# Kernel tuning notes

Measured on AMD Instinct MI355X. Metric: run time of the kernel, lower is better.

The kernel has to match this reference:

```python
import jax, jax.numpy as jnp
import numpy as np

B, H, W, C = 8, 64, 64, 64
DI = 2 * C   # d_inner = ssm_ratio * hidden_dim
N = 1        # ssm_d_state
K = 4        # scan directions
R = 4        # dt_rank = ceil(C/16)
EPS = 1e-5


def _ln(x, w, b):
    mu = x.mean(-1, keepdims=True)
    var = x.var(-1, keepdims=True)
    return (x - mu) / jnp.sqrt(var + EPS) * w + b


def _vss(x, p):
    (norm1_w, norm1_b, in_proj_w, conv_w, x_proj_w, dt_projs_w, dt_projs_b,
     A_logs, Ds, out_norm_w, out_norm_b, out_proj_w, norm2_w, norm2_b,
     fc1_w, fc1_b, fc2_w, fc2_b) = p
    # ---- SS2D branch (forward_type='v2') ----
    h = _ln(x, norm1_w, norm1_b)
    xz = h @ in_proj_w.T                      # (B,H,W,2*DI)
    xc, z = jnp.split(xz, 2, axis=-1)
    z = jax.nn.silu(z)
    xc = xc.transpose(0, 3, 1, 2)             # (B,DI,H,W)
    xc = jax.lax.conv_general_dilated(
        xc, conv_w, (1, 1), [(1, 1), (1, 1)], feature_group_count=DI,
        dimension_numbers=('NCHW', 'OIHW', 'NCHW'))  # depthwise 3x3, no bias
    xc = jax.nn.silu(xc)
    L = H * W
    # CrossScan: row-major, col-major, and their reverses
    x0 = xc.reshape(B, DI, L)
    x1 = xc.transpose(0, 1, 3, 2).reshape(B, DI, L)
    xs = jnp.stack([x0, x1, x0[..., ::-1], x1[..., ::-1]], axis=1)  # (B,K,DI,L)
    x_dbl = jnp.einsum('bkdl,kcd->bkcl', xs, x_proj_w)
    dts, Bs, Cs = x_dbl[:, :, :R], x_dbl[:, :, R:R + N], x_dbl[:, :, R + N:]
    delta = jax.nn.softplus(jnp.einsum('bkrl,kdr->bkdl', dts, dt_projs_w)
                            + dt_projs_b[None, :, :, None])          # (B,K,DI,L)
    A = -jnp.exp(A_logs).reshape(K, DI, N)
    # diagonal linear recurrence h_t = a_t*h_{t-1} + b_t via associative scan
    a = jnp.exp(delta[..., None] * A[None, :, :, None, :])           # (B,K,DI,L,N)
    b = delta[..., None] * Bs.transpose(0, 1, 3, 2)[:, :, None] * xs[..., None]
    def comb(c1, c2):
        a1, b1 = c1
        a2, b2 = c2
        return a1 * a2, b1 * a2 + b2
    _, hst = jax.lax.associative_scan(comb, (a, b), axis=3)          # (B,K,DI,L,N)
    ys = jnp.einsum('bkdln,bknl->bkdl', hst, Cs) \
         + Ds.reshape(K, DI)[None, :, :, None] * xs
    # CrossMerge
    ys = ys[:, :2] + ys[:, 2:, :, ::-1]
    y = ys[:, 0] + ys[:, 1].reshape(B, DI, W, H).transpose(0, 1, 3, 2).reshape(B, DI, L)
    y = y.transpose(0, 2, 1).reshape(B, H, W, DI)
    y = _ln(y, out_norm_w, out_norm_b)
    y = (y * z) @ out_proj_w.T
    x = x + y
    # ---- MLP branch ----
    h2 = _ln(x, norm2_w, norm2_b)
    h2 = jax.nn.gelu(h2 @ fc1_w.T + fc1_b, approximate=False)
    return x + (h2 @ fc2_w.T + fc2_b)


def setup_inputs():
    key = jax.random.key(0)
    ks = jax.random.split(key, 16)
    g = lambda i, shape, s=0.02: jax.random.normal(ks[i], shape, jnp.float32) * s
    return {
        'mag': jax.random.normal(ks[0], (B, H, W, C), jnp.float32),
        'phase': jax.random.normal(ks[1], (B, H, W, C), jnp.float32),
        'norm1_w': jnp.ones((2, C)), 'norm1_b': jnp.zeros((2, C)),
        'in_proj_w': g(2, (2, 2 * DI, C)),
        'conv_w': g(3, (2, DI, 1, 3, 3), 0.1),
        'x_proj_w': g(4, (2, K, R + 2 * N, DI)),
        'dt_projs_w': g(5, (2, K, DI, R), 0.1),
        'dt_projs_b': g(6, (2, K, DI), 0.1),
        'A_logs': g(7, (2, K * DI, N), 1.0),
        'Ds': jnp.ones((2, K * DI)),
        'out_norm_w': jnp.ones((2, DI)), 'out_norm_b': jnp.zeros((2, DI)),
        'out_proj_w': g(8, (2, C, DI)),
        'norm2_w': jnp.ones((2, C)), 'norm2_b': jnp.zeros((2, C)),
        'fc1_w': g(9, (2, 4 * C, C)), 'fc1_b': jnp.zeros((2, 4 * C)),
        'fc2_w': g(10, (2, C, 4 * C)), 'fc2_b': jnp.zeros((2, C)),
    }


def reference(mag, phase, norm1_w, norm1_b, in_proj_w, conv_w, x_proj_w,
              dt_projs_w, dt_projs_b, A_logs, Ds, out_norm_w, out_norm_b,
              out_proj_w, norm2_w, norm2_b, fc1_w, fc1_b, fc2_w, fc2_b):
    params = (norm1_w, norm1_b, in_proj_w, conv_w, x_proj_w, dt_projs_w,
              dt_projs_b, A_logs, Ds, out_norm_w, out_norm_b, out_proj_w,
              norm2_w, norm2_b, fc1_w, fc1_b, fc2_w, fc2_b)
    outs = jax.vmap(_vss)(jnp.stack([mag, phase]), params)  # branch dim = 2
    s = outs[0] + outs[1]
    return (s, s)
```

## Files before the change

kernel.cpp:

```cpp
#include <hip/hip_runtime.h>
#include <math.h>

#define LL   4096
#define DI   128
#define CC   64
#define BB   8
#define KK   4
#define LB   32768
#define NPIX 2097152
#define EPSF 1e-5f

#define OFF_XCIN   ((size_t)0)
#define OFF_XCONV  ((size_t)4194304)
#define OFF_XCONVT ((size_t)8388608)
#define OFF_Z      ((size_t)12582912)
#define OFF_Y      ((size_t)16777216)
#define OFF_YT     ((size_t)20971520)
#define OFF_XDBL   ((size_t)25165824)
#define ISTRIDE    ((size_t)25952256)
#define OFF_YCOMBT OFF_XCIN
#define OFF_XNEW   OFF_YT
#define OFF_SB     OFF_Y
#define OFF_WB     (OFF_Y + (size_t)2097152)
#define WB_IPW 0
#define WB_OPW 16384
#define WB_F1W 24576
#define WB_F2W 40960
#define WB_TOT 57344

typedef short v8s __attribute__((ext_vector_type(8)));
typedef float v4f __attribute__((ext_vector_type(4)));

__device__ __forceinline__ float fexp_(float x){ return __expf(x); }
__device__ __forceinline__ float silu_(float x){ return __fdividef(x, 1.f+__expf(-x)); }
__device__ __forceinline__ float softplusf_(float x){
  return fmaxf(x,0.f) + __logf(1.f + __expf(-fabsf(x)));
}
__device__ __forceinline__ float geluf_(float x){ return 0.5f*x*(1.f+erff(x*0.70710678118f)); }
__device__ __forceinline__ short bf16_(float x){
  unsigned u = __float_as_uint(x);
  u += 0x7FFF + ((u>>16)&1);
  return (short)(u>>16);
}
__device__ __forceinline__ float bf2f_(short s){
  return __uint_as_float(((unsigned)(unsigned short)s)<<16);
}

#define LD16(dst, ptr) { const float4* p4_=(const float4*)(ptr);                 \
  float4 v0_=p4_[0], v1_=p4_[1], v2_=p4_[2], v3_=p4_[3];                         \
  dst[0]=v0_.x; dst[1]=v0_.y; dst[2]=v0_.z; dst[3]=v0_.w;                        \
  dst[4]=v1_.x; dst[5]=v1_.y; dst[6]=v1_.z; dst[7]=v1_.w;                        \
  dst[8]=v2_.x; dst[9]=v2_.y; dst[10]=v2_.z; dst[11]=v2_.w;                      \
  dst[12]=v3_.x; dst[13]=v3_.y; dst[14]=v3_.z; dst[15]=v3_.w; }
#define LD16R(dst, ptr) { const float4* p4_=(const float4*)(ptr);                \
  float4 v0_=p4_[0], v1_=p4_[1], v2_=p4_[2], v3_=p4_[3];                         \
  dst[15]=v0_.x; dst[14]=v0_.y; dst[13]=v0_.z; dst[12]=v0_.w;                    \
  dst[11]=v1_.x; dst[10]=v1_.y; dst[9]=v1_.z;  dst[8]=v1_.w;                     \
  dst[7]=v2_.x;  dst[6]=v2_.y;  dst[5]=v2_.z;  dst[4]=v2_.w;                     \
  dst[3]=v3_.x;  dst[2]=v3_.y;  dst[1]=v3_.z;  dst[0]=v3_.w; }
#define LD16H(dst, ptr) { const v8s* p8_=(const v8s*)(ptr);                      \
  v8s a0_=p8_[0], a1_=p8_[1];                                                    \
  _Pragma("unroll") for(int e_=0;e_<8;++e_){ dst[e_]=bf2f_(a0_[e_]);             \
                                             dst[8+e_]=bf2f_(a1_[e_]); } }
#define ST16H(ptr, srcv) { v8s o0_, o1_;                                         \
  _Pragma("unroll") for(int e_=0;e_<8;++e_){ o0_[e_]=bf16_(srcv[e_]);            \
                                             o1_[e_]=bf16_(srcv[8+e_]); }        \
  ((v8s*)(ptr))[0]=o0_; ((v8s*)(ptr))[1]=o1_; }

__global__ __launch_bounds__(256) void kw_prep(
    const float* __restrict__ ipw_, const float* __restrict__ opw_,
    const float* __restrict__ f1w_, const float* __restrict__ f2w_,
    float* __restrict__ ws)
{
  const int i = blockIdx.y;
  short* wb = (short*)(ws + (size_t)i*ISTRIDE + OFF_WB);
  const int e0 = blockIdx.x*1024 + threadIdx.x;
  #pragma unroll
  for(int k=0;k<4;++k){
    const int e = e0 + k*256;
    float v;
    if(e < WB_OPW)      v = ipw_[(size_t)i*16384 + e];
    else if(e < WB_F1W) v = opw_[(size_t)i*8192  + (e - WB_OPW)];
    else if(e < WB_F2W) v = f1w_[(size_t)i*16384 + (e - WB_F1W)];
    else                v = f2w_[(size_t)i*16384 + (e - WB_F2W)];
    wb[e] = bf16_(v);
  }
}

__global__ __launch_bounds__(256) void k1_ln_inproj(
    const float* __restrict__ xmag, const float* __restrict__ xph,
    const float* __restrict__ n1w_, const float* __restrict__ n1b_,
    float* __restrict__ ws)
{
  const int i = blockIdx.y;
  const float* xin = i ? xph : xmag;
  const float* n1w = n1w_ + i*CC;
  const float* n1b = n1b_ + i*CC;
  float* base = ws + (size_t)i*ISTRIDE;
  const short* wb_ipw = (const short*)(base + OFF_WB) + WB_IPW;
  const int t = threadIdx.x, lane = t & 63;
  const int wv = __builtin_amdgcn_readfirstlane(t >> 6);
  const int m = lane & 15, quad = lane >> 4;
  const int p0 = blockIdx.x*64;
  const int b = p0 >> 12, l0 = p0 & (LL-1);

  __shared__ short hlds[64*72];
  __shared__ short w1lds[128*72];
  __shared__ float outs[128*68];

  {
    float hn[CC];
    const float* xr = xin + (size_t)(p0 + lane)*CC;
    LD16(hn, xr); LD16((hn+16), xr+16); LD16((hn+32), xr+32); LD16((hn+48), xr+48);
    float s1=0.f, s2=0.f;
    #pragma unroll
    for(int c=0;c<CC;++c){ s1 += hn[c]; s2 += hn[c]*hn[c]; }
    const float mu = s1*(1.f/CC);
    const float rs = rsqrtf(s2*(1.f/CC) - mu*mu + EPSF);
    if(wv==0){
      #pragma unroll
      for(int q=0;q<8;++q){
        v8s s;
        #pragma unroll
        for(int e=0;e<8;++e){
          const int c = q*8+e;
          s[e] = bf16_((hn[c]-mu)*rs*n1w[c] + n1b[c]);
        }
        *(v8s*)&hlds[lane*72 + q*8] = s;
      }
    }
  }

  for(int h=0; h<2; ++h){
    if(h) __syncthreads();
    {
      const int jl = t >> 1, hc = (t & 1)*32;
      const short* src = wb_ipw + (size_t)(h*128 + jl)*64 + hc;
      #pragma unroll
      for(int q=0;q<4;++q)
        *(v8s*)&w1lds[jl*72 + hc + q*8] = ((const v8s*)src)[q];
    }
    __syncthreads();
    #pragma unroll 2
    for(int nt=0; nt<8; ++nt){
      v4f acc = (v4f){0.f,0.f,0.f,0.f};
      #pragma unroll
      for(int ks=0; ks<2; ++ks){
        const v8s a = *(const v8s*)&hlds[(wv*16 + m)*72 + ks*32 + quad*8];
        const v8s bb = *(const v8s*)&w1lds[(nt*16 + m)*72 + ks*32 + quad*8];
        acc = __builtin_amdgcn_mfma_f32_16x16x32_bf16(a, bb, acc, 0, 0, 0);
      }
      *(float4*)&outs[(nt*16 + m)*68 + wv*16 + quad*4] =
          make_float4(acc[0], acc[1], acc[2], acc[3]);
    }
    __syncthreads();
    const int jl = t >> 1, hc = (t & 1)*32;
    if(h==0){
      short* xcb = (short*)(base + OFF_XCIN) + (size_t)b*DI*LL + (size_t)jl*LL + l0 + hc;
      const float* so = &outs[jl*68 + hc];
      ST16H(xcb, so);
      ST16H(xcb+16, (so+16));
    } else {
      short* zr = (short*)(base + OFF_Z) + (size_t)jl*LB + p0 + hc;
      float tmp[32];
      #pragma unroll
      for(int e=0;e<32;++e) tmp[e] = silu_(outs[jl*68 + hc + e]);
      ST16H(zr, tmp);
      ST16H(zr+16, (tmp+16));
    }
  }
}

__global__ __launch_bounds__(256) void k2_dwconv(
    const float* __restrict__ cw_, float* __restrict__ ws)
{
  const int i = blockIdx.y;
  const int bd = blockIdx.x;
  const int d = bd & (DI-1);
  const float* cw = cw_ + i*DI*9 + d*9;
  const short* xcin = (const short*)(ws + (size_t)i*ISTRIDE + OFF_XCIN) + (size_t)bd*LL;
  short* xconv  = (short*)(ws + (size_t)i*ISTRIDE + OFF_XCONV ) + (size_t)bd*LL;
  short* xconvT = (short*)(ws + (size_t)i*ISTRIDE + OFF_XCONVT) + (size_t)bd*LL;
  __shared__ float tin[64*65];
  __shared__ float tout[64*65];
  const int t = threadIdx.x;
  float w9[9];
  #pragma unroll
  for(int q=0;q<9;++q) w9[q] = cw[q];
  for(int idx=t; idx<4096; idx+=256)
    tin[(idx>>6)*65 + (idx&63)] = bf2f_(xcin[idx]);
  __syncthreads();
  const int w = t & 63, hb = (t>>6)*16;
  #pragma unroll
  for(int r=0;r<16;++r){
    const int h = hb + r;
    float acc = 0.f;
    #pragma unroll
    for(int dy=0;dy<3;++dy){
      const int hh = h + dy - 1;
      if(hh>=0 && hh<64){
        #pragma unroll
        for(int dx=0;dx<3;++dx){
          const int ww = w + dx - 1;
          if(ww>=0 && ww<64) acc += tin[hh*65+ww]*w9[dy*3+dx];
        }
      }
    }
    const float o = silu_(acc);
    tout[h*65+w] = o;
    xconv[h*64+w] = bf16_(o);
  }
  __syncthreads();
  const int hcol = t & 63, wb = (t>>6)*16;
  #pragma unroll
  for(int r=0;r<16;++r){
    const int wp = wb + r;
    xconvT[wp*64 + hcol] = bf16_(tout[hcol*65 + wp]);
  }
}

__global__ __launch_bounds__(256) void k3a_xproj(
    const float* __restrict__ xpw_, float* __restrict__ ws)
{
  const int i = blockIdx.z;
  const int b = blockIdx.y >> 1;
  const int kp = blockIdx.y & 1;
  const int l = blockIdx.x*256 + threadIdx.x;
  const short* src = (const short*)(ws + (size_t)i*ISTRIDE + (kp? OFF_XCONVT : OFF_XCONV))
                     + (size_t)b*DI*LL;
  const float* xpwF = xpw_ + i*KK*6*DI + kp*6*DI;
  const float* xpwB = xpw_ + i*KK*6*DI + (kp+2)*6*DI;
  float accF[6] = {0,0,0,0,0,0};
  float accB[6] = {0,0,0,0,0,0};
  for(int d=0; d<DI; ++d){
    const float xv = bf2f_(src[(size_t)d*LL + l]);
    #pragma unroll
    for(int c=0;c<6;++c){
      accF[c] += xv * xpwF[c*DI + d];
      accB[c] += xv * xpwB[c*DI + d];
    }
  }
  float* xdF = (ws + (size_t)i*ISTRIDE + OFF_XDBL) + (size_t)(b*KK+kp  )*6*LL;
  float* xdB = (ws + (size_t)i*ISTRIDE + OFF_XDBL) + (size_t)(b*KK+kp+2)*6*LL;
  #pragma unroll
  for(int c=0;c<6;++c) xdF[(size_t)c*LL + l] = accF[c];
  #pragma unroll
  for(int c=0;c<6;++c) xdB[(size_t)c*LL + (LL-1-l)] = accB[c];
}

__global__ __launch_bounds__(256,3) void k3b_scan(
    const float* __restrict__ dtw_, const float* __restrict__ dtb_,
    const float* __restrict__ alog_, const float* __restrict__ Ds_,
    float* __restrict__ ws)
{
  const int gid = blockIdx.x;
  const int i = blockIdx.y;
  const int d  = gid & (DI-1);
  const int b  = gid >> 7;
  const int t = threadIdx.x, lane = t & 63, wv = t >> 6;
  float* base = ws + (size_t)i*ISTRIDE;
  const int l0 = t*16;
  const int s0 = LL - 16 - l0;

  __shared__ float tile[64*65];
  __shared__ float wAg[4], wBg[4], vAg[4], vBg[4];

  #pragma unroll 1
  for(int kp=0; kp<2; ++kp){
    const short* src = (const short*)(base + (kp? OFF_XCONVT : OFF_XCONV)) + (size_t)(b*DI+d)*LL;
    const float* xdF = (base + OFF_XDBL) + (size_t)(b*KK+kp  )*6*LL;
    const float* xdB = (base + OFF_XDBL) + (size_t)(b*KK+kp+2)*6*LL;
    const int kdF = kp*DI + d, kdB = (kp+2)*DI + d;
    const float4 wF = ((const float4*)dtw_)[i*KK*DI + kdF];
    const float4 wB = ((const float4*)dtw_)[i*KK*DI + kdB];
    const float biasF = dtb_[i*KK*DI + kdF], biasB = dtb_[i*KK*DI + kdB];
    const float AvF = -fexp_(alog_[i*KK*DI + kdF]);
    const float AvB = -fexp_(alog_[i*KK*DI + kdB]);
    const float Dsum = Ds_[i*KK*DI + kdF] + Ds_[i*KK*DI + kdB];

    float vX[16], aF[16], bF[16], aB[16], bB[16];
    float fA = 1.f, fB = 0.f, gA = 1.f, gB = 0.f;
    LD16H(vX, src + l0);

    {
      float pre[16], r0[16];
      LD16(r0, xdF + 0*LL + l0);
      #pragma unroll
      for(int j=0;j<16;++j) pre[j] = biasF + wF.x*r0[j];
      LD16(r0, xdF + 1*LL + l0);
      #pragma unroll
      for(int j=0;j<16;++j) pre[j] += wF.y*r0[j];
      LD16(r0, xdF + 2*LL + l0);
      #pragma unroll
      for(int j=0;j<16;++j) pre[j] += wF.z*r0[j];
      LD16(r0, xdF + 3*LL + l0);
      #pragma unroll
      for(int j=0;j<16;++j) pre[j] += wF.w*r0[j];
      LD16(r0, xdF + 4*LL + l0);
      #pragma unroll
      for(int j=0;j<16;++j){
        const float delta = softplusf_(pre[j]);
        aF[j] = fexp_(delta*AvF);
        bF[j] = delta*r0[j]*vX[j];
        fB = fB*aF[j] + bF[j];
        fA *= aF[j];
      }
    }
    {
      float pre[16], r0[16];
      LD16R(r0, xdB + 0*LL + s0);
      #pragma unroll
      for(int j=0;j<16;++j) pre[j] = biasB + wB.x*r0[j];
      LD16R(r0, xdB + 1*LL + s0);
      #pragma unroll
      for(int j=0;j<16;++j) pre[j] += wB.y*r0[j];
      LD16R(r0, xdB + 2*LL + s0);
      #pragma unroll
      for(int j=0;j<16;++j) pre[j] += wB.z*r0[j];
      LD16R(r0, xdB + 3*LL + s0);
      #pragma unroll
      for(int j=0;j<16;++j) pre[j] += wB.w*r0[j];
      LD16R(r0, xdB + 4*LL + s0);
      #pragma unroll
      for(int j=15;j>=0;--j){
        const float delta = softplusf_(pre[j]);
        aB[j] = fexp_(delta*AvB);
        bB[j] = delta*r0[j]*vX[j];
        gB = gB*aB[j] + bB[j];
        gA *= aB[j];
      }
    }

    #pragma unroll
    for(int off=1; off<64; off<<=1){
      const float aL = __shfl_up(fA, off);
      const float bL = __shfl_up(fB, off);
      if(lane >= off){ fB = bL*fA + fB; fA = aL*fA; }
    }
    float pA = __shfl_up(fA, 1), pB = __shfl_up(fB, 1);
    if(lane==0){ pA=1.f; pB=0.f; }
    #pragma unroll
    for(int off=1; off<64; off<<=1){
      const float aR = __shfl_down(gA, off);
      const float bR = __shfl_down(gB, off);
      if(lane + off < 64){ gB = gA*bR + gB; gA = gA*aR; }
    }
    float qA = __shfl_down(gA, 1), qB = __shfl_down(gB, 1);
    if(lane==63){ qA=1.f; qB=0.f; }

    if(kp) __syncthreads();
    if(lane==63){ wAg[wv]=fA; wBg[wv]=fB; }
    if(lane==0){ vAg[wv]=gA; vBg[wv]=gB; }
    __syncthreads();
    float eB=0.f;
    for(int u=0; u<wv; ++u){ eB = wAg[u]*eB + wBg[u]; }
    float rB=0.f;
    for(int u=3; u>wv; --u){ rB = vAg[u]*rB + vBg[u]; }

    float hf = pA*eB + pB;
    float hb = qA*rB + qB;

    float out[16], cc[16];
    LD16(cc, xdF + 5*LL + l0);
    #pragma unroll
    for(int j=0;j<16;++j){
      hf = aF[j]*hf + bF[j];
      out[j] = hf*cc[j] + Dsum*vX[j];
    }
    LD16R(cc, xdB + 5*LL + s0);
    #pragma unroll
    for(int j=15;j>=0;--j){
      hb = aB[j]*hb + bB[j];
      out[j] += hb*cc[j];
    }

    if(kp==0){
      #pragma unroll
      for(int j=0;j<16;++j){
        const int l = l0 + j;
        tile[(l>>6)*65 + (l&63)] = out[j];
      }
    } else {
      #pragma unroll
      for(int j=0;j<16;++j){
        const int q = l0 + j;
        tile[(q&63)*65 + (q>>6)] += out[j];
      }
    }
  }

  __syncthreads();
  {
    short* ycT = (short*)(base + OFF_YCOMBT);
    float o[16];
    #pragma unroll
    for(int j=0;j<16;++j)
      o[j] = tile[(t>>2)*65 + (t&3)*16 + j];
    ST16H(ycT + (size_t)d*LB + b*LL + l0, o);
  }
}

__global__ __launch_bounds__(256) void k4a_proj(
    const float* __restrict__ xmag, const float* __restrict__ xph,
    const float* __restrict__ onw_, const float* __restrict__ onb_,
    float* __restrict__ ws)
{
  const int i = blockIdx.y;
  const float* xin = i ? xph : xmag;
  const float* onw = onw_ + i*DI;
  const float* onb = onb_ + i*DI;
  float* base = ws + (size_t)i*ISTRIDE;
  const short* ycT = (const short*)(base + OFF_YCOMBT);
  const short* zT  = (const short*)(base + OFF_Z);
  const short* wb  = (const short*)(base + OFF_WB);
  const int t = threadIdx.x, lane = t & 63;
  const int wv = __builtin_amdgcn_readfirstlane(t >> 6);
  const int m = lane & 15, quad = lane >> 4;
  const int p0 = blockIdx.x*64;
  const int p = p0 + lane;

  __shared__ short ynlds[64*136];
  __shared__ short wlds[64*136];
  __shared__ float st[64][9];

  float yv[32];
  float s1=0.f, s2=0.f;
  #pragma unroll 8
  for(int c=0;c<32;++c){
    const float v = bf2f_(ycT[(size_t)(wv*32+c)*LB + p]);
    yv[c]=v; s1+=v; s2+=v*v;
  }
  st[lane][wv*2]=s1; st[lane][wv*2+1]=s2;
  __syncthreads();
  const float S1 = st[lane][0]+st[lane][2]+st[lane][4]+st[lane][6];
  const float S2 = st[lane][1]+st[lane][3]+st[lane][5]+st[lane][7];
  const float mu = S1*(1.f/DI);
  const float rs = rsqrtf(S2*(1.f/DI) - mu*mu + EPSF);
  #pragma unroll
  for(int cq=0;cq<8;++cq){
    short4 s4;
    #pragma unroll
    for(int e=0;e<4;++e){
      const int c = cq*4+e;
      const int d = wv*32 + c;
      ((short*)&s4)[e] = bf16_(((yv[c]-mu)*rs*onw[d] + onb[d]) * bf2f_(zT[(size_t)d*LB + p]));
    }
    *(short4*)&ynlds[lane*136 + wv*32 + cq*4] = s4;
  }
  {
    const int ol = t >> 2, seg = (t & 3)*32;
    const short* src = wb + WB_OPW + (size_t)ol*DI + seg;
    #pragma unroll
    for(int q=0;q<4;++q)
      *(v8s*)&wlds[ol*136 + seg + q*8] = ((const v8s*)src)[q];
  }
  __syncthreads();

  v4f accs[4];
  #pragma unroll
  for(int nt=0; nt<4; ++nt){
    v4f acc = (v4f){0.f,0.f,0.f,0.f};
    #pragma unroll
    for(int ks=0; ks<4; ++ks){
      const v8s a = *(const v8s*)&ynlds[(wv*16 + m)*136 + ks*32 + quad*8];
      const v8s b = *(const v8s*)&wlds[(nt*16 + m)*136 + ks*32 + quad*8];
      acc = __builtin_amdgcn_mfma_f32_16x16x32_bf16(a, b, acc, 0, 0, 0);
    }
    accs[nt] = acc;
  }
  short* xnew = (short*)(base + OFF_XNEW);
  #pragma unroll
  for(int nt=0; nt<4; ++nt){
    #pragma unroll
    for(int r=0;r<4;++r){
      const int pp = p0 + wv*16 + quad*4 + r;
      const int o = nt*16 + m;
      xnew[(size_t)pp*CC + o] = bf16_(accs[nt][r] + xin[(size_t)pp*CC + o]);
    }
  }
}

__global__ __launch_bounds__(256) void k4b_mlp(
    const float* __restrict__ n2w_, const float* __restrict__ n2b_,
    const float* __restrict__ f1b_, const float* __restrict__ f2b_,
    float* __restrict__ ws)
{
  const int i = blockIdx.y;
  const float* n2w = n2w_ + i*CC;
  const float* n2b = n2b_ + i*CC;
  const float* f1b = f1b_ + i*256;
  const float* f2b = f2b_ + i*CC;
  float* base = ws + (size_t)i*ISTRIDE;
  const short* xnew = (const short*)(base + OFF_XNEW);
  const short* wb   = (const short*)(base + OFF_WB);
  const int t = threadIdx.x, lane = t & 63;
  const int wv = __builtin_amdgcn_readfirstlane(t >> 6);
  const int m = lane & 15, quad = lane >> 4;
  const int p0 = blockIdx.x*64;

  __shared__ short hlds[64*72];
  __shared__ short w1lds[128*72];
  __shared__ short glds[64*136];
  __shared__ short w2lds[64*136];

  {
    float h2[64];
    const short* xr = xnew + (size_t)(p0 + lane)*CC;
    LD16H(h2, xr); LD16H((h2+16), xr+16); LD16H((h2+32), xr+32); LD16H((h2+48), xr+48);
    float s1=0.f, s2=0.f;
    #pragma unroll
    for(int c=0;c<CC;++c){ s1 += h2[c]; s2 += h2[c]*h2[c]; }
    const float mu = s1*(1.f/CC);
    const float rs = rsqrtf(s2*(1.f/CC) - mu*mu + EPSF);
    if(wv==0){
      #pragma unroll
      for(int q=0;q<8;++q){
        v8s s;
        #pragma unroll
        for(int e=0;e<8;++e){
          const int c = q*8+e;
          s[e] = bf16_((h2[c]-mu)*rs*n2w[c] + n2b[c]);
        }
        *(v8s*)&hlds[lane*72 + q*8] = s;
      }
    }
  }

  v4f acc2[4];
  #pragma unroll
  for(int n=0;n<4;++n) acc2[n] = (v4f){0.f,0.f,0.f,0.f};

  for(int h=0; h<2; ++h){
    if(h) __syncthreads();
    {
      const int jl = t >> 1, hc = (t & 1)*32;
      const short* src = wb + WB_F1W + (size_t)(h*128 + jl)*64 + hc;
      #pragma unroll
      for(int q=0;q<4;++q)
        *(v8s*)&w1lds[jl*72 + hc + q*8] = ((const v8s*)src)[q];
    }
    {
      const int ol = t >> 2, seg = (t & 3)*32;
      const short* src = wb + WB_F2W + (size_t)ol*256 + h*128 + seg;
      #pragma unroll
      for(int q=0;q<4;++q)
        *(v8s*)&w2lds[ol*136 + seg + q*8] = ((const v8s*)src)[q];
    }
    __syncthreads();
    #pragma unroll 2
    for(int nt=0; nt<8; ++nt){
      v4f acc = (v4f){0.f,0.f,0.f,0.f};
      #pragma unroll
      for(int ks=0; ks<2; ++ks){
        const v8s a = *(const v8s*)&hlds[(wv*16 + m)*72 + ks*32 + quad*8];
        const v8s b = *(const v8s*)&w1lds[(nt*16 + m)*72 + ks*32 + quad*8];
        acc = __builtin_amdgcn_mfma_f32_16x16x32_bf16(a, b, acc, 0, 0, 0);
      }
      const float bj = f1b[h*128 + nt*16 + m];
      #pragma unroll
      for(int r=0;r<4;++r){
        glds[(wv*16 + quad*4 + r)*136 + nt*16 + m] = bf16_(geluf_(acc[r] + bj));
      }
    }
    #pragma unroll
    for(int nt=0; nt<4; ++nt){
      v4f acc = acc2[nt];
      #pragma unroll
      for(int ks=0; ks<4; ++ks){
        const v8s a = *(const v8s*)&glds[(wv*16 + m)*136 + ks*32 + quad*8];
        const v8s b = *(const v8s*)&w2lds[(nt*16 + m)*136 + ks*32 + quad*8];
        acc = __builtin_amdgcn_mfma_f32_16x16x32_bf16(a, b, acc, 0, 0, 0);
      }
      acc2[nt] = acc;
    }
  }

  short* sb = (short*)(base + OFF_SB);
  #pragma unroll
  for(int nt=0; nt<4; ++nt){
    const float bo = f2b[nt*16 + m];
    #pragma unroll
    for(int r=0;r<4;++r){
      const int p = p0 + wv*16 + quad*4 + r;
      const int o = nt*16 + m;
      sb[(size_t)p*CC + o] = bf16_(acc2[nt][r] + bo + bf2f_(xnew[(size_t)p*CC + o]));
    }
  }
}

__global__ __launch_bounds__(256) void k5_final(
    const float* __restrict__ ws, float* __restrict__ out)
{
  const int idx = blockIdx.x*256 + threadIdx.x;
  const v8s a = ((const v8s*)(ws + OFF_SB))[idx];
  const v8s b = ((const v8s*)(ws + ISTRIDE + OFF_SB))[idx];
  float4 v0, v1;
  v0.x = bf2f_(a[0])+bf2f_(b[0]); v0.y = bf2f_(a[1])+bf2f_(b[1]);
  v0.z = bf2f_(a[2])+bf2f_(b[2]); v0.w = bf2f_(a[3])+bf2f_(b[3]);
  v1.x = bf2f_(a[4])+bf2f_(b[4]); v1.y = bf2f_(a[5])+bf2f_(b[5]);
  v1.z = bf2f_(a[6])+bf2f_(b[6]); v1.w = bf2f_(a[7])+bf2f_(b[7]);
  ((float4*)out)[idx*2]   = v0;
  ((float4*)out)[idx*2+1] = v1;
  ((float4*)out)[NPIX/4 + idx*2]   = v0;
  ((float4*)out)[NPIX/4 + idx*2+1] = v1;
}

extern "C" void kernel_launch(void* const* d_in, const int* in_sizes, int n_in,
                              void* d_out, int out_size, void* d_ws, size_t ws_size,
                              hipStream_t stream)
{
  const float* mag  = (const float*)d_in[0];
  const float* ph   = (const float*)d_in[1];
  const float* n1w  = (const float*)d_in[2];
  const float* n1b  = (const float*)d_in[3];
  const float* ipw  = (const float*)d_in[4];
  const float* cw   = (const float*)d_in[5];
  const float* xpw  = (const float*)d_in[6];
  const float* dtw  = (const float*)d_in[7];
  const float* dtb  = (const float*)d_in[8];
  const float* alog = (const float*)d_in[9];
  const float* Ds   = (const float*)d_in[10];
  const float* onw  = (const float*)d_in[11];
  const float* onb  = (const float*)d_in[12];
  const float* opw  = (const float*)d_in[13];
  const float* n2w  = (const float*)d_in[14];
  const float* n2b  = (const float*)d_in[15];
  const float* f1w  = (const float*)d_in[16];
  const float* f1b  = (const float*)d_in[17];
  const float* f2w  = (const float*)d_in[18];
  const float* f2b  = (const float*)d_in[19];
  float* ws = (float*)d_ws;
  float* out = (float*)d_out;

  kw_prep     <<<dim3(56,2),   256, 0, stream>>>(ipw, opw, f1w, f2w, ws);
  k1_ln_inproj<<<dim3(512,2),  256, 0, stream>>>(mag, ph, n1w, n1b, ws);
  k2_dwconv   <<<dim3(1024,2), 256, 0, stream>>>(cw, ws);
  k3a_xproj   <<<dim3(16,16,2),256, 0, stream>>>(xpw, ws);
  k3b_scan    <<<dim3(1024,2), 256, 0, stream>>>(dtw, dtb, alog, Ds, ws);
  k4a_proj    <<<dim3(512,2),  256, 0, stream>>>(mag, ph, onw, onb, ws);
  k4b_mlp     <<<dim3(512,2),  256, 0, stream>>>(n2w, n2b, f1b, f2b, ws);
  k5_final    <<<dim3(1024),   256, 0, stream>>>(ws, out);
}
```

Baseline: 289.6 us.

## Store x_dbl in bf16 and fuse branch sum into MLP kernel

The x-projection output (dt, B, C coefficients) is now stored as bf16 instead of fp32, which halves the traffic between k3a_xproj and the scan kernel. The MLP kernel now loops over both branches inside one block, adds their results in registers and writes both output copies directly. This removes the bf16 intermediate buffer and the separate final-sum kernel launch. In exchange, the bf16 coefficients cost precision, and the MLP grid is halved (512 blocks), each doing twice the serial work.

```diff
diff --git a/kernel.cpp b/kernel.cpp
--- a/kernel.cpp
+++ b/kernel.cpp
@@ -20,7 +20,6 @@
 #define ISTRIDE    ((size_t)25952256)
 #define OFF_YCOMBT OFF_XCIN
 #define OFF_XNEW   OFF_YT
-#define OFF_SB     OFF_Y
 #define OFF_WB     (OFF_Y + (size_t)2097152)
 #define WB_IPW 0
 #define WB_OPW 16384
@@ -52,16 +51,14 @@
   dst[4]=v1_.x; dst[5]=v1_.y; dst[6]=v1_.z; dst[7]=v1_.w;                        \
   dst[8]=v2_.x; dst[9]=v2_.y; dst[10]=v2_.z; dst[11]=v2_.w;                      \
   dst[12]=v3_.x; dst[13]=v3_.y; dst[14]=v3_.z; dst[15]=v3_.w; }
-#define LD16R(dst, ptr) { const float4* p4_=(const float4*)(ptr);                \
-  float4 v0_=p4_[0], v1_=p4_[1], v2_=p4_[2], v3_=p4_[3];                         \
-  dst[15]=v0_.x; dst[14]=v0_.y; dst[13]=v0_.z; dst[12]=v0_.w;                    \
-  dst[11]=v1_.x; dst[10]=v1_.y; dst[9]=v1_.z;  dst[8]=v1_.w;                     \
-  dst[7]=v2_.x;  dst[6]=v2_.y;  dst[5]=v2_.z;  dst[4]=v2_.w;                     \
-  dst[3]=v3_.x;  dst[2]=v3_.y;  dst[1]=v3_.z;  dst[0]=v3_.w; }
 #define LD16H(dst, ptr) { const v8s* p8_=(const v8s*)(ptr);                      \
   v8s a0_=p8_[0], a1_=p8_[1];                                                    \
   _Pragma("unroll") for(int e_=0;e_<8;++e_){ dst[e_]=bf2f_(a0_[e_]);             \
                                              dst[8+e_]=bf2f_(a1_[e_]); } }
+#define LD16HR(dst, ptr) { const v8s* p8_=(const v8s*)(ptr);                     \
+  v8s a0_=p8_[0], a1_=p8_[1];                                                    \
+  _Pragma("unroll") for(int e_=0;e_<8;++e_){ dst[15-e_]=bf2f_(a0_[e_]);          \
+                                             dst[7-e_]=bf2f_(a1_[e_]); } }
 #define ST16H(ptr, srcv) { v8s o0_, o1_;                                         \
   _Pragma("unroll") for(int e_=0;e_<8;++e_){ o0_[e_]=bf16_(srcv[e_]);            \
                                              o1_[e_]=bf16_(srcv[8+e_]); }        \
@@ -240,12 +237,12 @@
       accB[c] += xv * xpwB[c*DI + d];
     }
   }
-  float* xdF = (ws + (size_t)i*ISTRIDE + OFF_XDBL) + (size_t)(b*KK+kp  )*6*LL;
-  float* xdB = (ws + (size_t)i*ISTRIDE + OFF_XDBL) + (size_t)(b*KK+kp+2)*6*LL;
-  #pragma unroll
-  for(int c=0;c<6;++c) xdF[(size_t)c*LL + l] = accF[c];
-  #pragma unroll
-  for(int c=0;c<6;++c) xdB[(size_t)c*LL + (LL-1-l)] = accB[c];
+  short* xdF = (short*)(ws + (size_t)i*ISTRIDE + OFF_XDBL) + (size_t)(b*KK+kp  )*6*LL;
+  short* xdB = (short*)(ws + (size_t)i*ISTRIDE + OFF_XDBL) + (size_t)(b*KK+kp+2)*6*LL;
+  #pragma unroll
+  for(int c=0;c<6;++c) xdF[(size_t)c*LL + l] = bf16_(accF[c]);
+  #pragma unroll
+  for(int c=0;c<6;++c) xdB[(size_t)c*LL + (LL-1-l)] = bf16_(accB[c]);
 }
 
 __global__ __launch_bounds__(256,3) void k3b_scan(
@@ -268,8 +265,8 @@
   #pragma unroll 1
   for(int kp=0; kp<2; ++kp){
     const short* src = (const short*)(base + (kp? OFF_XCONVT : OFF_XCONV)) + (size_t)(b*DI+d)*LL;
-    const float* xdF = (base + OFF_XDBL) + (size_t)(b*KK+kp  )*6*LL;
-    const float* xdB = (base + OFF_XDBL) + (size_t)(b*KK+kp+2)*6*LL;
+    const short* xdF = (const short*)(base + OFF_XDBL) + (size_t)(b*KK+kp  )*6*LL;
+    const short* xdB = (const short*)(base + OFF_XDBL) + (size_t)(b*KK+kp+2)*6*LL;
     const int kdF = kp*DI + d, kdB = (kp+2)*DI + d;
     const float4 wF = ((const float4*)dtw_)[i*KK*DI + kdF];
     const float4 wB = ((const float4*)dtw_)[i*KK*DI + kdB];
@@ -284,19 +281,19 @@
 
     {
       float pre[16], r0[16];
-      LD16(r0, xdF + 0*LL + l0);
+      LD16H(r0, xdF + 0*LL + l0);
       #pragma unroll
       for(int j=0;j<16;++j) pre[j] = biasF + wF.x*r0[j];
-      LD16(r0, xdF + 1*LL + l0);
+      LD16H(r0, xdF + 1*LL + l0);
       #pragma unroll
       for(int j=0;j<16;++j) pre[j] += wF.y*r0[j];
-      LD16(r0, xdF + 2*LL + l0);
+      LD16H(r0, xdF + 2*LL + l0);
       #pragma unroll
       for(int j=0;j<16;++j) pre[j] += wF.z*r0[j];
-      LD16(r0, xdF + 3*LL + l0);
+      LD16H(r0, xdF + 3*LL + l0);
       #pragma unroll
       for(int j=0;j<16;++j) pre[j] += wF.w*r0[j];
-      LD16(r0, xdF + 4*LL + l0);
+      LD16H(r0, xdF + 4*LL + l0);
       #pragma unroll
       for(int j=0;j<16;++j){
         const float delta = softplusf_(pre[j]);
@@ -308,19 +305,19 @@
     }
     {
       float pre[16], r0[16];
-      LD16R(r0, xdB + 0*LL + s0);
+      LD16HR(r0, xdB + 0*LL + s0);
       #pragma unroll
       for(int j=0;j<16;++j) pre[j] = biasB + wB.x*r0[j];
-      LD16R(r0, xdB + 1*LL + s0);
+      LD16HR(r0, xdB + 1*LL + s0);
       #pragma unroll
       for(int j=0;j<16;++j) pre[j] += wB.y*r0[j];
-      LD16R(r0, xdB + 2*LL + s0);
+      LD16HR(r0, xdB + 2*LL + s0);
       #pragma unroll
       for(int j=0;j<16;++j) pre[j] += wB.z*r0[j];
-      LD16R(r0, xdB + 3*LL + s0);
+      LD16HR(r0, xdB + 3*LL + s0);
       #pragma unroll
       for(int j=0;j<16;++j) pre[j] += wB.w*r0[j];
-      LD16R(r0, xdB + 4*LL + s0);
+      LD16HR(r0, xdB + 4*LL + s0);
       #pragma unroll
       for(int j=15;j>=0;--j){
         const float delta = softplusf_(pre[j]);
@@ -361,13 +358,13 @@
     float hb = qA*rB + qB;
 
     float out[16], cc[16];
-    LD16(cc, xdF + 5*LL + l0);
+    LD16H(cc, xdF + 5*LL + l0);
     #pragma unroll
     for(int j=0;j<16;++j){
       hf = aF[j]*hf + bF[j];
       out[j] = hf*cc[j] + Dsum*vX[j];
     }
-    LD16R(cc, xdB + 5*LL + s0);
+    LD16HR(cc, xdB + 5*LL + s0);
     #pragma unroll
     for(int j=15;j>=0;--j){
       hb = aB[j]*hb + bB[j];
@@ -483,16 +480,8 @@
 __global__ __launch_bounds__(256) void k4b_mlp(
     const float* __restrict__ n2w_, const float* __restrict__ n2b_,
     const float* __restrict__ f1b_, const float* __restrict__ f2b_,
-    float* __restrict__ ws)
-{
-  const int i = blockIdx.y;
-  const float* n2w = n2w_ + i*CC;
-  const float* n2b = n2b_ + i*CC;
-  const float* f1b = f1b_ + i*256;
-  const float* f2b = f2b_ + i*CC;
-  float* base = ws + (size_t)i*ISTRIDE;
-  const short* xnew = (const short*)(base + OFF_XNEW);
-  const short* wb   = (const short*)(base + OFF_WB);
+    float* __restrict__ ws, float* __restrict__ out)
+{
   const int t = threadIdx.x, lane = t & 63;
   const int wv = __builtin_amdgcn_readfirstlane(t >> 6);
   const int m = lane & 15, quad = lane >> 4;
@@ -503,106 +492,116 @@
   __shared__ short glds[64*136];
   __shared__ short w2lds[64*136];
 
-  {
-    float h2[64];
-    const short* xr = xnew + (size_t)(p0 + lane)*CC;
-    LD16H(h2, xr); LD16H((h2+16), xr+16); LD16H((h2+32), xr+32); LD16H((h2+48), xr+48);
-    float s1=0.f, s2=0.f;
-    #pragma unroll
-    for(int c=0;c<CC;++c){ s1 += h2[c]; s2 += h2[c]*h2[c]; }
-    const float mu = s1*(1.f/CC);
-    const float rs = rsqrtf(s2*(1.f/CC) - mu*mu + EPSF);
-    if(wv==0){
-      #pragma unroll
-      for(int q=0;q<8;++q){
-        v8s s;
-        #pragma unroll
-        for(int e=0;e<8;++e){
-          const int c = q*8+e;
-          s[e] = bf16_((h2[c]-mu)*rs*n2w[c] + n2b[c]);
+  float outsum[16];
+  #pragma unroll
+  for(int e=0;e<16;++e) outsum[e]=0.f;
+
+  #pragma unroll 1
+  for(int i=0;i<2;++i){
+    float* base = ws + (size_t)i*ISTRIDE;
+    const short* xnew = (const short*)(base + OFF_XNEW);
+    const short* wb   = (const short*)(base + OFF_WB);
+    const float* n2w = n2w_ + i*CC;
+    const float* n2b = n2b_ + i*CC;
+    const float* f1b = f1b_ + i*256;
+    const float* f2b = f2b_ + i*CC;
+
+    if(i) __syncthreads();
+
+    {
+      float h2[64];
+      const short* xr = xnew + (size_t)(p0 + lane)*CC;
+      LD16H(h2, xr); LD16H((h2+16), xr+16); LD16H((h2+32), xr+32); LD16H((h2+48), xr+48);
+      float s1=0.f, s2=0.f;
+      #pragma unroll
+      for(int c=0;c<CC;++c){ s1 += h2[c]; s2 += h2[c]*h2[c]; }
+      const float mu = s1*(1.f/CC);
+      const float rs = rsqrtf(s2*(1.f/CC) - mu*mu + EPSF);
+      if(wv==0){
+        #pragma unroll
+        for(int q=0;q<8;++q){
+          v8s s;
+          #pragma unroll
+          for(int e=0;e<8;++e){
+            const int c = q*8+e;
+            s[e] = bf16_((h2[c]-mu)*rs*n2w[c] + n2b[c]);
+          }
+          *(v8s*)&hlds[lane*72 + q*8] = s;
         }
-        *(v8s*)&hlds[lane*72 + q*8] = s;
-      }
-    }
-  }
-
-  v4f acc2[4];
-  #pragma unroll
-  for(int n=0;n<4;++n) acc2[n] = (v4f){0.f,0.f,0.f,0.f};
-
-  for(int h=0; h<2; ++h){
-    if(h) __syncthreads();
-    {
-      const int jl = t >> 1, hc = (t & 1)*32;
-      const short* src = wb + WB_F1W + (size_t)(h*128 + jl)*64 + hc;
-      #pragma unroll
-      for(int q=0;q<4;++q)
-        *(v8s*)&w1lds[jl*72 + hc + q*8] = ((const v8s*)src)[q];
-    }
-    {
-      const int ol = t >> 2, seg = (t & 3)*32;
-      const short* src = wb + WB_F2W + (size_t)ol*256 + h*128 + seg;
-      #pragma unroll
-      for(int q=0;q<4;++q)
-        *(v8s*)&w2lds[ol*136 + seg + q*8] = ((const v8s*)src)[q];
-    }
-    __syncthreads();
-    #pragma unroll 2
-    for(int nt=0; nt<8; ++nt){
-      v4f acc = (v4f){0.f,0.f,0.f,0.f};
-      #pragma unroll
-      for(int ks=0; ks<2; ++ks){
-        const v8s a = *(const v8s*)&hlds[(wv*16 + m)*72 + ks*32 + quad*8];
-        const v8s b = *(const v8s*)&w1lds[(nt*16 + m)*72 + ks*32 + quad*8];
-        acc = __builtin_amdgcn_mfma_f32_16x16x32_bf16(a, b, acc, 0, 0, 0);
-      }
-      const float bj = f1b[h*128 + nt*16 + m];
+      }
+    }
+
+    v4f acc2[4];
+    #pragma unroll
+    for(int n=0;n<4;++n) acc2[n] = (v4f){0.f,0.f,0.f,0.f};
+
+    for(int h=0; h<2; ++h){
+      if(h) __syncthreads();
+      {
+        const int jl = t >> 1, hc = (t & 1)*32;
+        const short* src = wb + WB_F1W + (size_t)(h*128 + jl)*64 + hc;
+        #pragma unroll
+        for(int q=0;q<4;++q)
+          *(v8s*)&w1lds[jl*72 + hc + q*8] = ((const v8s*)src)[q];
+      }
+      {
+        const int ol = t >> 2, seg = (t & 3)*32;
+        const short* src = wb + WB_F2W + (size_t)ol*256 + h*128 + seg;
+        #pragma unroll
+        for(int q=0;q<4;++q)
+          *(v8s*)&w2lds[ol*136 + seg + q*8] = ((const v8s*)src)[q];
+      }
+      __syncthreads();
+      #pragma unroll 2
+      for(int nt=0; nt<8; ++nt){
+        v4f acc = (v4f){0.f,0.f,0.f,0.f};
+        #pragma unroll
+        for(int ks=0; ks<2; ++ks){
+          const v8s a = *(const v8s*)&hlds[(wv*16 + m)*72 + ks*32 + quad*8];
+          const v8s b = *(const v8s*)&w1lds[(nt*16 + m)*72 + ks*32 + quad*8];
+          acc = __builtin_amdgcn_mfma_f32_16x16x32_bf16(a, b, acc, 0, 0, 0);
+        }
+        const float bj = f1b[h*128 + nt*16 + m];
+        #pragma unroll
+        for(int r=0;r<4;++r){
+          glds[(wv*16 + quad*4 + r)*136 + nt*16 + m] = bf16_(geluf_(acc[r] + bj));
+        }
+      }
+      #pragma unroll
+      for(int nt=0; nt<4; ++nt){
+        v4f acc = acc2[nt];
+        #pragma unroll
+        for(int ks=0; ks<4; ++ks){
+          const v8s a = *(const v8s*)&glds[(wv*16 + m)*136 + ks*32 + quad*8];
+          const v8s b = *(const v8s*)&w2lds[(nt*16 + m)*136 + ks*32 + quad*8];
+          acc = __builtin_amdgcn_mfma_f32_16x16x32_bf16(a, b, acc, 0, 0, 0);
+        }
+        acc2[nt] = acc;
+      }
+    }
+
+    #pragma unroll
+    for(int nt=0; nt<4; ++nt){
+      const float bo = f2b[nt*16 + m];
       #pragma unroll
       for(int r=0;r<4;++r){
-        glds[(wv*16 + quad*4 + r)*136 + nt*16 + m] = bf16_(geluf_(acc[r] + bj));
-      }
-    }
-    #pragma unroll
-    for(int nt=0; nt<4; ++nt){
-      v4f acc = acc2[nt];
-      #pragma unroll
-      for(int ks=0; ks<4; ++ks){
-        const v8s a = *(const v8s*)&glds[(wv*16 + m)*136 + ks*32 + quad*8];
-        const v8s b = *(const v8s*)&w2lds[(nt*16 + m)*136 + ks*32 + quad*8];
-        acc = __builtin_amdgcn_mfma_f32_16x16x32_bf16(a, b, acc, 0, 0, 0);
-      }
-      acc2[nt] = acc;
-    }
-  }
-
-  short* sb = (short*)(base + OFF_SB);
+        const int pp = p0 + wv*16 + quad*4 + r;
+        const int o  = nt*16 + m;
+        outsum[nt*4+r] += acc2[nt][r] + bo + bf2f_(xnew[(size_t)pp*CC + o]);
+      }
+    }
+  }
+
   #pragma unroll
   for(int nt=0; nt<4; ++nt){
-    const float bo = f2b[nt*16 + m];
     #pragma unroll
     for(int r=0;r<4;++r){
-      const int p = p0 + wv*16 + quad*4 + r;
-      const int o = nt*16 + m;
-      sb[(size_t)p*CC + o] = bf16_(acc2[nt][r] + bo + bf2f_(xnew[(size_t)p*CC + o]));
-    }
-  }
-}
-
-__global__ __launch_bounds__(256) void k5_final(
-    const float* __restrict__ ws, float* __restrict__ out)
-{
-  const int idx = blockIdx.x*256 + threadIdx.x;
-  const v8s a = ((const v8s*)(ws + OFF_SB))[idx];
-  const v8s b = ((const v8s*)(ws + ISTRIDE + OFF_SB))[idx];
-  float4 v0, v1;
-  v0.x = bf2f_(a[0])+bf2f_(b[0]); v0.y = bf2f_(a[1])+bf2f_(b[1]);
-  v0.z = bf2f_(a[2])+bf2f_(b[2]); v0.w = bf2f_(a[3])+bf2f_(b[3]);
-  v1.x = bf2f_(a[4])+bf2f_(b[4]); v1.y = bf2f_(a[5])+bf2f_(b[5]);
-  v1.z = bf2f_(a[6])+bf2f_(b[6]); v1.w = bf2f_(a[7])+bf2f_(b[7]);
-  ((float4*)out)[idx*2]   = v0;
-  ((float4*)out)[idx*2+1] = v1;
-  ((float4*)out)[NPIX/4 + idx*2]   = v0;
-  ((float4*)out)[NPIX/4 + idx*2+1] = v1;
+      const int pp = p0 + wv*16 + quad*4 + r;
+      const int o  = nt*16 + m;
+      out[(size_t)pp*CC + o] = outsum[nt*4+r];
+      out[(size_t)NPIX + (size_t)pp*CC + o] = outsum[nt*4+r];
+    }
+  }
 }
 
 extern "C" void kernel_launch(void* const* d_in, const int* in_sizes, int n_in,
@@ -638,6 +637,5 @@
   k3a_xproj   <<<dim3(16,16,2),256, 0, stream>>>(xpw, ws);
   k3b_scan    <<<dim3(1024,2), 256, 0, stream>>>(dtw, dtb, alog, Ds, ws);
   k4a_proj    <<<dim3(512,2),  256, 0, stream>>>(mag, ph, onw, onb, ws);
-  k4b_mlp     <<<dim3(512,2),  256, 0, stream>>>(n2w, n2b, f1b, f2b, ws);
-  k5_final    <<<dim3(1024),   256, 0, stream>>>(ws, out);
-}
+  k4b_mlp     <<<dim3(512),    256, 0, stream>>>(n2w, n2b, f1b, f2b, ws, out);
+}
```

New measurement: 261.0 us. 1.11x faster.
